# Optimization experiments

Hardware: AMD Instinct MI355X
Metric: run time of the kernel (lower is better)

Reference implementation:

```python
import jax, jax.numpy as jnp
import numpy as np
from jax import lax

B, CIN, H, W = 8, 256, 64, 64
CC = 128          # corr_channels
COUT = 64         # out_channels
KH = KW = 5       # corr_kernel_size
SH = SW = 1       # corr_stride
PT, PB = KH // 2, (KH + 1) // 2 - 1   # pad='k'
PL, PR = KW // 2, (KW + 1) // 2 - 1


def setup_inputs() -> dict:
    key = jax.random.key(0)
    k1, k2, k3, k4, k5 = jax.random.split(key, 5)
    x = jax.random.normal(k1, (B, CIN, H, W), dtype=jnp.float32)
    w_ext = jax.random.normal(k2, (CC, CIN, 3, 3), dtype=jnp.float32) * 0.02
    b_ext = jax.random.normal(k3, (CC,), dtype=jnp.float32) * 0.02
    w_reg = jax.random.normal(k4, (COUT, CC, KH, KW), dtype=jnp.float32) * 0.02
    b_reg = jax.random.normal(k5, (COUT,), dtype=jnp.float32) * 0.02
    return {"x": x, "w_ext": w_ext, "b_ext": b_ext, "w_reg": w_reg, "b_reg": b_reg}


def _forward(x, w_ext, b_ext, w_reg, b_reg):
    # feature extraction: 3x3 conv, padding 1
    f = lax.conv_general_dilated(x, w_ext, (1, 1), ((1, 1), (1, 1)))
    f = f + b_ext[None, :, None, None]
    # local autocorrelation: multiply each window element by the window center, per channel
    fp = jnp.pad(f, ((0, 0), (0, 0), (PT, PB), (PL, PR)))
    nH = (fp.shape[2] - KH) // SH + 1
    nW = (fp.shape[3] - KW) // SW + 1
    center = fp[:, :, KH // 2:KH // 2 + nH * SH:SH, KW // 2:KW // 2 + nW * SW:SW]  # [B,CC,nH,nW]
    patches = jnp.stack(
        [fp[:, :, u:u + nH * SH:SH, v:v + nW * SW:SW] for u in range(KH) for v in range(KW)],
        axis=-1)  # [B,CC,nH,nW,KH*KW]
    corr = patches * center[..., None]  # [B,CC,nH,nW,KH*KW]
    out = jnp.einsum('bcijk,ock->bijo', corr, w_reg.reshape(COUT, CC, KH * KW))
    out = out + b_reg
    return out.transpose(0, 3, 1, 2)  # permute=True -> [B, COUT, nH, nW]


def reference(x, w_ext, b_ext, w_reg, b_reg):
    return _forward(x, w_ext, b_ext, w_reg, b_reg)
```

## Files before the change

kernel.cpp:

```cpp
#include <hip/hip_runtime.h>
#include <hip/hip_bf16.h>

#define B_    8
#define CIN_  256
#define CC_   128
#define COUT_ 64
#define HP_   68
#define HPX_  (HP_ * HP_)
#define XQW_  66
#define XQPX_ (XQW_ * XQW_)

typedef __attribute__((ext_vector_type(8))) short bh8;
typedef __attribute__((ext_vector_type(4))) float f4;

__device__ __forceinline__ ushort f2bf(float f) {
    uint u = __float_as_uint(f);
    return (ushort)((u + 0x7fffu + ((u >> 16) & 1u)) >> 16);
}
__device__ __forceinline__ float bf2f(ushort s) {
    return __uint_as_float(((uint)s) << 16);
}
__device__ __forceinline__ short f2bf_c(float f) {
    __hip_bfloat16 h = __float2bfloat16(f);
    short s;
    __builtin_memcpy(&s, &h, 2);
    return s;
}

#define NB_MISC 2217
__global__ __launch_bounds__(256) void prep_all(const float* __restrict__ x,
                                                const float* __restrict__ w_ext,
                                                const float* __restrict__ w_reg,
                                                short* __restrict__ wg,
                                                short* __restrict__ wa,
                                                ushort* __restrict__ fpad_t,
                                                ushort* __restrict__ xq) {
    __shared__ float xt[2][32][65];
    const int tid = threadIdx.x;
    if (blockIdx.x < NB_MISC) {
        int e = blockIdx.x * 256 + tid;
        if (e < 67584) {
            int seg = e & 15;
            int t = e >> 4;
            int b = t / 528, rp = t - b * 528;
            int i, j;
            if (rp < 136) { i = rp / 68; j = rp - (rp / 68) * 68; }
            else if (rp < 272) { int r = rp - 136; i = 66 + r / 68; j = r - (r / 68) * 68; }
            else { int r = rp - 272; i = 2 + (r >> 2); int c = r & 3; j = (c < 2) ? c : c + 64; }
            uint4 z; z.x = 0u; z.y = 0u; z.z = 0u; z.w = 0u;
            *(uint4*)&fpad_t[(((size_t)b * HPX_) + i * HP_ + j) * 128 + seg * 8] = z;
            return;
        }
        e -= 67584;
        if (e < 294912) {
            int ci = e & 31;
            int t  = e >> 5;
            int cc = t & 127;
            int t2 = t >> 7;
            int rs = t2 % 9, cb = t2 / 9;
            wg[e] = (short)f2bf(w_ext[(cc * CIN_ + cb * 32 + ci) * 9 + rs]);
            return;
        }
        e -= 294912;
        if (e < 204800) {
            int ci = e & 31;
            int o  = (e >> 5) & 63;
            int rest = e >> 11;
            int k = rest % 25, q = rest / 25;
            wa[e] = (short)f2bf(w_reg[(o * CC_ + q * 32 + ci) * 25 + k]);
        }
        return;
    }

    const int pid = blockIdx.x - NB_MISC;
    const int rp = pid % 33, cb = (pid / 33) & 7, b = pid / 264;

#pragma unroll
    for (int rr = 0; rr < 2; ++rr) {
        int y = rp * 2 + rr - 1;
        if ((unsigned)y < 64u) {
            int xx = tid & 63, wv = tid >> 6;
#pragma unroll
            for (int it = 0; it < 8; ++it) {
                int ci = it * 4 + wv;
                xt[rr][ci][xx] = x[(((size_t)(b * CIN_ + cb * 32 + ci)) * 64 + y) * 64 + xx];
            }
        }
    }
    __syncthreads();

    for (int e = tid; e < 528; e += 256) {
        int rr = e / 264, t = e - rr * 264;
        int hc = t >> 2, seg = t & 3;
        int y = rp * 2 + rr - 1, xx = hc - 1;
        uint pk[4] = {0u, 0u, 0u, 0u};
        if ((unsigned)y < 64u && (unsigned)xx < 64u) {
#pragma unroll
            for (int i = 0; i < 4; ++i) {
                uint lo = f2bf(xt[rr][seg * 8 + i * 2][xx]);
                uint hi = f2bf(xt[rr][seg * 8 + i * 2 + 1][xx]);
                pk[i] = lo | (hi << 16);
            }
        }
        uint4 v; v.x = pk[0]; v.y = pk[1]; v.z = pk[2]; v.w = pk[3];
        *(uint4*)&xq[((((size_t)(b * 8 + cb)) * XQPX_) + (rp * 2 + rr) * XQW_ + hc) * 32 + seg * 8] = v;
    }
}

__device__ __forceinline__ void stage_xq(const ushort* __restrict__ xq, short* __restrict__ dst,
                                         int b, int cb, int i0, int j0, int tid) {
    const ushort* base = xq + (((size_t)(b * 8 + cb)) * XQPX_) * 32;
    for (int e = tid; e < 400; e += 256) {
        int hp = e >> 2, seg = e & 3;
        int hr = hp / 10, hc = hp - hr * 10;
        const ushort* src = base + ((size_t)((i0 + hr) * XQW_ + (j0 + hc))) * 32 + seg * 8;
        *(bh8*)&dst[hp * 72 + seg * 8] = *(const bh8*)src;
    }
}

__global__ __launch_bounds__(256)
__attribute__((amdgpu_waves_per_eu(2, 2)))
void conv3x3_mfma(const ushort* __restrict__ xq,
                  const short* __restrict__ wg,
                  const float* __restrict__ bext,
                  ushort* __restrict__ fpad_t) {
    __shared__ __align__(16) short xh[2][100 * 72];
    const int tid = threadIdx.x;
    const int lane = tid & 63, wv = tid >> 6;
    const int j0 = blockIdx.x * 8, i0 = blockIdx.y * 8, b = blockIdx.z;
    const int l15 = lane & 15, kg = lane >> 4;
    const int cc0 = wv * 32;

    f4 acc[2][4] = {};

    stage_xq(xq, xh[0], b, 0, i0, j0, tid);
    __syncthreads();

    for (int cb = 0; cb < 8; ++cb) {
        const int buf = cb & 1;
        if (cb < 7) stage_xq(xq, xh[buf ^ 1], b, cb + 1, i0, j0, tid);

        const short* wbase = wg + (size_t)(cb * 9) * 128 * 32;
        bh8 a[9][2];
#pragma unroll
        for (int rs = 0; rs < 9; ++rs)
#pragma unroll
            for (int mm = 0; mm < 2; ++mm)
                a[rs][mm] = *(const bh8*)(wbase + (rs * 128 + cc0 + mm * 16 + l15) * 32 + kg * 8);

#pragma unroll
        for (int rs = 0; rs < 9; ++rs) {
            const int r = rs / 3, s = rs % 3;
            bh8 bb[4];
#pragma unroll
            for (int nn = 0; nn < 4; ++nn) {
                int px = nn * 16 + l15, pi = px >> 3, pj = px & 7;
                int hidx = (pi + r) * 10 + (pj + s);
                bb[nn] = *(const bh8*)&xh[buf][hidx * 72 + kg * 8];
            }
#pragma unroll
            for (int mm = 0; mm < 2; ++mm)
#pragma unroll
                for (int nn = 0; nn < 4; ++nn)
                    acc[mm][nn] = __builtin_amdgcn_mfma_f32_16x16x32_bf16(
                        a[rs][mm], bb[nn], acc[mm][nn], 0, 0, 0);
        }
        __syncthreads();
    }

#pragma unroll
    for (int mm = 0; mm < 2; ++mm) {
        const int ccb = cc0 + mm * 16 + kg * 4;
        float bv0 = bext[ccb + 0], bv1 = bext[ccb + 1];
        float bv2 = bext[ccb + 2], bv3 = bext[ccb + 3];
#pragma unroll
        for (int nn = 0; nn < 4; ++nn) {
            int px = nn * 16 + l15, pi = px >> 3, pj = px & 7;
            size_t row = (size_t)b * HPX_ + (2 + i0 + pi) * HP_ + (2 + j0 + pj);
            uint lo = (uint)f2bf(acc[mm][nn][0] + bv0) | ((uint)f2bf(acc[mm][nn][1] + bv1) << 16);
            uint hi = (uint)f2bf(acc[mm][nn][2] + bv2) | ((uint)f2bf(acc[mm][nn][3] + bv3) << 16);
            uint2 pk; pk.x = lo; pk.y = hi;
            *(uint2*)&fpad_t[row * 128 + ccb] = pk;
        }
    }
}

__global__ __launch_bounds__(256)
__attribute__((amdgpu_waves_per_eu(2, 2)))
void autocorr_mfma(const ushort* __restrict__ ft,
                   const short* __restrict__ wA,
                   const float* __restrict__ breg,
                   float* __restrict__ out) {
    __shared__ __align__(16) short flds[144 * 136];
    const int tid = threadIdx.x;
    const int lane = tid & 63, wv = tid >> 6;
    const int oh = wv >> 1, ph = wv & 1;
    const int j0 = blockIdx.x * 8, i0 = blockIdx.y * 8, b = blockIdx.z;
    const int l15 = lane & 15, kg = lane >> 4;

    for (int e = tid; e < 2304; e += 256) {
        int hp = e >> 4, seg = e & 15;
        int hr = hp / 12, hc = hp - hr * 12;
        const ushort* src = ft + ((size_t)b * HPX_ + (i0 + hr) * HP_ + (j0 + hc)) * 128 + seg * 8;
        *(bh8*)&flds[hp * 136 + seg * 8] = *(const bh8*)src;
    }
    __syncthreads();

    f4 acc[2][2] = {};
    int base_off[2], cen_off[2];
#pragma unroll
    for (int t = 0; t < 2; ++t) {
        int px = ph * 32 + t * 16 + l15;
        int pi = px >> 3, pj = px & 7;
        base_off[t] = (pi * 12 + pj) * 136 + kg * 8;
        cen_off[t]  = ((pi + 2) * 12 + (pj + 2)) * 136 + kg * 8;
    }

#pragma unroll 1
    for (int q = 0; q < 4; ++q) {
        float cen[2][8];
#pragma unroll
        for (int t = 0; t < 2; ++t) {
            bh8 c8 = *(const bh8*)&flds[cen_off[t] + q * 32];
#pragma unroll
            for (int jj = 0; jj < 8; ++jj) cen[t][jj] = bf2f((ushort)c8[jj]);
        }
        const short* wq = wA + q * (25 * 64 * 32);
#pragma unroll
        for (int u = 0; u < 5; ++u) {
            bh8 a[5][2];
#pragma unroll
            for (int v = 0; v < 5; ++v)
#pragma unroll
                for (int mm = 0; mm < 2; ++mm)
                    a[v][mm] = *(const bh8*)(wq + ((u * 5 + v) * 64 + oh * 32 + mm * 16 + l15) * 32 + kg * 8);

#pragma unroll
            for (int v = 0; v < 5; ++v) {
                const int koff = (u * 12 + v) * 136;
                bh8 bb[2];
#pragma unroll
                for (int t = 0; t < 2; ++t) {
                    bh8 s8 = *(const bh8*)&flds[base_off[t] + q * 32 + koff];
#pragma unroll
                    for (int jj = 0; jj < 8; ++jj) {
                        float p = bf2f((ushort)s8[jj]) * cen[t][jj];
                        bb[t][jj] = f2bf_c(p);
                    }
                }
#pragma unroll
                for (int mm = 0; mm < 2; ++mm)
#pragma unroll
                    for (int t = 0; t < 2; ++t)
                        acc[mm][t] = __builtin_amdgcn_mfma_f32_16x16x32_bf16(
                            a[v][mm], bb[t], acc[mm][t], 0, 0, 0);
            }
        }
    }

#pragma unroll
    for (int mm = 0; mm < 2; ++mm) {
#pragma unroll
        for (int reg = 0; reg < 4; ++reg) {
            int o = oh * 32 + mm * 16 + kg * 4 + reg;
            float bv = breg[o];
#pragma unroll
            for (int t = 0; t < 2; ++t) {
                int px = ph * 32 + t * 16 + l15, pi = px >> 3, pj = px & 7;
                out[(((size_t)(b * COUT_ + o)) * 64 + i0 + pi) * 64 + j0 + pj] =
                    acc[mm][t][reg] + bv;
            }
        }
    }
}

extern "C" void kernel_launch(void* const* d_in, const int* in_sizes, int n_in,
                              void* d_out, int out_size, void* d_ws, size_t ws_size,
                              hipStream_t stream) {
    const float* x     = (const float*)d_in[0];
    const float* w_ext = (const float*)d_in[1];
    const float* b_ext = (const float*)d_in[2];
    const float* w_reg = (const float*)d_in[3];
    const float* b_reg = (const float*)d_in[4];
    float* out = (float*)d_out;

    char* ws = (char*)d_ws;
    const size_t FPADT_BYTES = (size_t)B_ * HPX_ * 128 * 2;
    const size_t WG_BYTES    = (size_t)8 * 9 * 128 * 32 * 2;
    const size_t WA_BYTES    = (size_t)4 * 25 * 64 * 32 * 2;
    ushort* fpad_t = (ushort*)ws;
    short*  wgq    = (short*)(ws + FPADT_BYTES);
    short*  wa     = (short*)(ws + FPADT_BYTES + WG_BYTES);
    ushort* xq     = (ushort*)(ws + FPADT_BYTES + WG_BYTES + WA_BYTES);

    prep_all<<<NB_MISC + 33 * 8 * 8, 256, 0, stream>>>(x, w_ext, w_reg, wgq, wa, fpad_t, xq);

    dim3 grid(8, 8, 8);
    conv3x3_mfma<<<grid, 256, 0, stream>>>(xq, wgq, b_ext, fpad_t);
    autocorr_mfma<<<grid, 256, 0, stream>>>(fpad_t, wa, b_reg, out);
}
```

Measured before the change: 87.12 us.

## Stage weights through double-buffered swizzled LDS in conv and autocorr kernels

Both MFMA kernels now load weight slices cooperatively into double-buffered, XOR-swizzled shared memory instead of each wave reading its own fragments straight from global memory. The next weight slice (and, in the conv kernel, the next input-channel block) is prefetched into registers while MFMAs run on the current buffer, then written to LDS before a barrier. This replaces redundant per-wave global weight traffic and large register arrays with shared reuse and software pipelining. The cost is more barriers (24 and 20 per block) and extra LDS, which may reduce occupancy.

```diff
diff --git a/kernel.cpp b/kernel.cpp
--- a/kernel.cpp
+++ b/kernel.cpp
@@ -107,17 +107,6 @@
     }
 }
 
-__device__ __forceinline__ void stage_xq(const ushort* __restrict__ xq, short* __restrict__ dst,
-                                         int b, int cb, int i0, int j0, int tid) {
-    const ushort* base = xq + (((size_t)(b * 8 + cb)) * XQPX_) * 32;
-    for (int e = tid; e < 400; e += 256) {
-        int hp = e >> 2, seg = e & 3;
-        int hr = hp / 10, hc = hp - hr * 10;
-        const ushort* src = base + ((size_t)((i0 + hr) * XQW_ + (j0 + hc))) * 32 + seg * 8;
-        *(bh8*)&dst[hp * 72 + seg * 8] = *(const bh8*)src;
-    }
-}
-
 __global__ __launch_bounds__(256)
 __attribute__((amdgpu_waves_per_eu(2, 2)))
 void conv3x3_mfma(const ushort* __restrict__ xq,
@@ -125,47 +114,108 @@
                   const float* __restrict__ bext,
                   ushort* __restrict__ fpad_t) {
     __shared__ __align__(16) short xh[2][100 * 72];
+    __shared__ __align__(16) short wlds[2][3 * 128 * 32];
     const int tid = threadIdx.x;
     const int lane = tid & 63, wv = tid >> 6;
     const int j0 = blockIdx.x * 8, i0 = blockIdx.y * 8, b = blockIdx.z;
     const int l15 = lane & 15, kg = lane >> 4;
     const int cc0 = wv * 32;
 
+    int abase[2];
+#pragma unroll
+    for (int mm = 0; mm < 2; ++mm) {
+        int cc = cc0 + mm * 16 + l15;
+        abase[mm] = cc * 32 + ((((cc >> 1) + kg) & 3) << 3);
+    }
+    int xb[4];
+#pragma unroll
+    for (int nn = 0; nn < 4; ++nn) {
+        int px = nn * 16 + l15, pi = px >> 3, pj = px & 7;
+        xb[nn] = (pi * 10 + pj) * 72 + kg * 8;
+    }
+    int wdst[6]; int goff[6];
+#pragma unroll
+    for (int k = 0; k < 6; ++k) {
+        int c = tid + k * 256;
+        int cc = (c & 511) >> 2, kgc = c & 3;
+        wdst[k] = (c >> 9) * 4096 + cc * 32 + ((((cc >> 1) + kgc) & 3) << 3);
+        goff[k] = c * 8;
+    }
+    const int hp0 = tid >> 2, seg0 = tid & 3;
+    const int hr0 = hp0 / 10, hc0 = hp0 - hr0 * 10;
+    const int xsrc0 = ((i0 + hr0) * XQW_ + (j0 + hc0)) * 32 + seg0 * 8;
+    const int xdst0 = hp0 * 72 + seg0 * 8;
+    const int hp1 = (tid + 256) >> 2;
+    const int hr1 = hp1 / 10, hc1 = hp1 - hr1 * 10;
+    const int xsrc1 = ((i0 + hr1) * XQW_ + (j0 + hc1)) * 32 + seg0 * 8;
+    const int xdst1 = hp1 * 72 + seg0 * 8;
+    const bool x1ok = tid < 144;
+
     f4 acc[2][4] = {};
 
-    stage_xq(xq, xh[0], b, 0, i0, j0, tid);
+    {
+#pragma unroll
+        for (int k = 0; k < 6; ++k)
+            *(bh8*)&wlds[0][wdst[k]] = *(const bh8*)(wg + goff[k]);
+        const ushort* xbase = xq + (((size_t)(b * 8 + 0)) * XQPX_) * 32;
+        *(bh8*)&xh[0][xdst0] = *(const bh8*)&xbase[xsrc0];
+        if (x1ok) *(bh8*)&xh[0][xdst1] = *(const bh8*)&xbase[xsrc1];
+    }
     __syncthreads();
 
+    int p = 0;
+#pragma unroll 1
     for (int cb = 0; cb < 8; ++cb) {
-        const int buf = cb & 1;
-        if (cb < 7) stage_xq(xq, xh[buf ^ 1], b, cb + 1, i0, j0, tid);
-
-        const short* wbase = wg + (size_t)(cb * 9) * 128 * 32;
-        bh8 a[9][2];
-#pragma unroll
-        for (int rs = 0; rs < 9; ++rs)
-#pragma unroll
-            for (int mm = 0; mm < 2; ++mm)
-                a[rs][mm] = *(const bh8*)(wbase + (rs * 128 + cc0 + mm * 16 + l15) * 32 + kg * 8);
-
-#pragma unroll
-        for (int rs = 0; rs < 9; ++rs) {
-            const int r = rs / 3, s = rs % 3;
-            bh8 bb[4];
-#pragma unroll
-            for (int nn = 0; nn < 4; ++nn) {
-                int px = nn * 16 + l15, pi = px >> 3, pj = px & 7;
-                int hidx = (pi + r) * 10 + (pj + s);
-                bb[nn] = *(const bh8*)&xh[buf][hidx * 72 + kg * 8];
-            }
-#pragma unroll
-            for (int mm = 0; mm < 2; ++mm)
+        const int xbuf = cb & 1;
+#pragma unroll 1
+        for (int g = 0; g < 3; ++g) {
+            const int buf = p & 1;
+            const bool wmore = (p < 23);
+            const bool xmore = (g == 2) && (cb < 7);
+
+            bh8 wreg[6];
+            const short* gsrc = wg + (size_t)(wmore ? (p + 1) : 23) * 12288;
+#pragma unroll
+            for (int k = 0; k < 6; ++k)
+                wreg[k] = *(const bh8*)(gsrc + goff[k]);
+            bh8 xr0, xr1;
+            if (xmore) {
+                const ushort* xbase = xq + (((size_t)(b * 8 + cb + 1)) * XQPX_) * 32;
+                xr0 = *(const bh8*)&xbase[xsrc0];
+                if (x1ok) xr1 = *(const bh8*)&xbase[xsrc1];
+            }
+
+            const short* wb = wlds[buf];
+            const int goffs = g * 10 * 72;
+#pragma unroll
+            for (int s = 0; s < 3; ++s) {
+                bh8 a[2], bb[4];
+#pragma unroll
+                for (int mm = 0; mm < 2; ++mm)
+                    a[mm] = *(const bh8*)&wb[s * 4096 + abase[mm]];
 #pragma unroll
                 for (int nn = 0; nn < 4; ++nn)
-                    acc[mm][nn] = __builtin_amdgcn_mfma_f32_16x16x32_bf16(
-                        a[rs][mm], bb[nn], acc[mm][nn], 0, 0, 0);
-        }
-        __syncthreads();
+                    bb[nn] = *(const bh8*)&xh[xbuf][xb[nn] + goffs + s * 72];
+#pragma unroll
+                for (int mm = 0; mm < 2; ++mm)
+#pragma unroll
+                    for (int nn = 0; nn < 4; ++nn)
+                        acc[mm][nn] = __builtin_amdgcn_mfma_f32_16x16x32_bf16(
+                            a[mm], bb[nn], acc[mm][nn], 0, 0, 0);
+            }
+
+            if (wmore) {
+#pragma unroll
+                for (int k = 0; k < 6; ++k)
+                    *(bh8*)&wlds[buf ^ 1][wdst[k]] = wreg[k];
+            }
+            if (xmore) {
+                *(bh8*)&xh[xbuf ^ 1][xdst0] = xr0;
+                if (x1ok) *(bh8*)&xh[xbuf ^ 1][xdst1] = xr1;
+            }
+            __syncthreads();
+            ++p;
+        }
     }
 
 #pragma unroll
@@ -192,18 +242,37 @@
                    const float* __restrict__ breg,
                    float* __restrict__ out) {
     __shared__ __align__(16) short flds[144 * 136];
+    __shared__ __align__(16) short wlds[2][5 * 64 * 32];
     const int tid = threadIdx.x;
     const int lane = tid & 63, wv = tid >> 6;
     const int oh = wv >> 1, ph = wv & 1;
     const int j0 = blockIdx.x * 8, i0 = blockIdx.y * 8, b = blockIdx.z;
     const int l15 = lane & 15, kg = lane >> 4;
 
+    int abase[2];
+#pragma unroll
+    for (int mm = 0; mm < 2; ++mm) {
+        int o = oh * 32 + mm * 16 + l15;
+        abase[mm] = o * 32 + ((((o >> 1) + kg) & 3) << 3);
+    }
+    int wdst[5]; int goff[5];
+#pragma unroll
+    for (int k = 0; k < 5; ++k) {
+        int c = tid + k * 256;
+        int o = (c & 255) >> 2, kgc = c & 3;
+        wdst[k] = (c >> 8) * 2048 + o * 32 + ((((o >> 1) + kgc) & 3) << 3);
+        goff[k] = c * 8;
+    }
+
     for (int e = tid; e < 2304; e += 256) {
         int hp = e >> 4, seg = e & 15;
         int hr = hp / 12, hc = hp - hr * 12;
         const ushort* src = ft + ((size_t)b * HPX_ + (i0 + hr) * HP_ + (j0 + hc)) * 128 + seg * 8;
         *(bh8*)&flds[hp * 136 + seg * 8] = *(const bh8*)src;
     }
+#pragma unroll
+    for (int k = 0; k < 5; ++k)
+        *(bh8*)&wlds[0][wdst[k]] = *(const bh8*)(wA + goff[k]);
     __syncthreads();
 
     f4 acc[2][2] = {};
@@ -216,6 +285,7 @@
         cen_off[t]  = ((pi + 2) * 12 + (pj + 2)) * 136 + kg * 8;
     }
 
+    int p = 0;
 #pragma unroll 1
     for (int q = 0; q < 4; ++q) {
         float cen[2][8];
@@ -225,27 +295,33 @@
 #pragma unroll
             for (int jj = 0; jj < 8; ++jj) cen[t][jj] = bf2f((ushort)c8[jj]);
         }
-        const short* wq = wA + q * (25 * 64 * 32);
-#pragma unroll
+#pragma unroll 1
         for (int u = 0; u < 5; ++u) {
-            bh8 a[5][2];
-#pragma unroll
-            for (int v = 0; v < 5; ++v)
-#pragma unroll
-                for (int mm = 0; mm < 2; ++mm)
-                    a[v][mm] = *(const bh8*)(wq + ((u * 5 + v) * 64 + oh * 32 + mm * 16 + l15) * 32 + kg * 8);
-
+            const int buf = p & 1;
+            const bool wmore = (p < 19);
+
+            bh8 wreg[5];
+            const short* gsrc = wA + (size_t)(wmore ? (p + 1) : 19) * 10240;
+#pragma unroll
+            for (int k = 0; k < 5; ++k)
+                wreg[k] = *(const bh8*)(gsrc + goff[k]);
+
+            const short* wb = wlds[buf];
 #pragma unroll
             for (int v = 0; v < 5; ++v) {
                 const int koff = (u * 12 + v) * 136;
+                bh8 a[2];
+#pragma unroll
+                for (int mm = 0; mm < 2; ++mm)
+                    a[mm] = *(const bh8*)&wb[v * 2048 + abase[mm]];
                 bh8 bb[2];
 #pragma unroll
                 for (int t = 0; t < 2; ++t) {
                     bh8 s8 = *(const bh8*)&flds[base_off[t] + q * 32 + koff];
 #pragma unroll
                     for (int jj = 0; jj < 8; ++jj) {
-                        float p = bf2f((ushort)s8[jj]) * cen[t][jj];
-                        bb[t][jj] = f2bf_c(p);
+                        float pr = bf2f((ushort)s8[jj]) * cen[t][jj];
+                        bb[t][jj] = f2bf_c(pr);
                     }
                 }
 #pragma unroll
@@ -253,8 +329,16 @@
 #pragma unroll
                     for (int t = 0; t < 2; ++t)
                         acc[mm][t] = __builtin_amdgcn_mfma_f32_16x16x32_bf16(
-                            a[v][mm], bb[t], acc[mm][t], 0, 0, 0);
-            }
+                            a[mm], bb[t], acc[mm][t], 0, 0, 0);
+            }
+
+            if (wmore) {
+#pragma unroll
+                for (int k = 0; k < 5; ++k)
+                    *(bh8*)&wlds[buf ^ 1][wdst[k]] = wreg[k];
+            }
+            __syncthreads();
+            ++p;
         }
     }
 
```

New measurement: 77.41 us. 11.1% less time.
